# Optimization experiments

Measured on AMD Instinct MI355X. Metric: run time of the kernel, lower is better.

## Reference

```python
import jax, jax.numpy as jnp
import numpy as np

B, S, DIM = 2, 2048, 2048
NH, NKV = 32, 8
HD = DIM // NH  # 64


def setup_inputs() -> dict:
    key = jax.random.key(0)
    ks = jax.random.split(key, 6)
    x = jax.random.normal(ks[0], (B, S, DIM), jnp.float32)
    # realistic rotary tables: [S, HD//2]
    inv_freq = 1.0 / (10000.0 ** (jnp.arange(0, HD, 2, dtype=jnp.float32) / HD))
    freqs = jnp.arange(S, dtype=jnp.float32)[:, None] * inv_freq[None, :]
    cos, sin = jnp.cos(freqs), jnp.sin(freqs)
    init = lambda k, shape: jax.random.normal(k, shape, jnp.float32) * (shape[0] ** -0.5)
    Wq = init(ks[1], (DIM, NH * HD))
    Wk = init(ks[2], (DIM, NKV * HD))
    Wv = init(ks[3], (DIM, NKV * HD))
    Wo = init(ks[4], (NH * HD, DIM))
    return {"x": x, "cos": cos, "sin": sin, "Wq": Wq, "Wk": Wk, "Wv": Wv, "Wo": Wo}


def _rope(t, c, s):
    # t: [B, S, H, HD]; c, s: [1, S, 1, HD//2]; consecutive-pair (v1) style
    b, sl, h, hd = t.shape
    tp = t.reshape(b, sl, h, hd // 2, 2)
    t0, t1 = tp[..., 0], tp[..., 1]
    return jnp.stack([t0 * c - t1 * s, t0 * s + t1 * c], axis=-1).reshape(b, sl, h, hd)


def reference(x, cos, sin, Wq, Wk, Wv, Wo):
    b, sl, _ = x.shape
    q = (x @ Wq).reshape(b, sl, NH, HD)
    k = (x @ Wk).reshape(b, sl, NKV, HD)
    v = (x @ Wv).reshape(b, sl, NKV, HD)
    c = cos[None, :, None, :]
    s = sin[None, :, None, :]
    q = _rope(q, c, s)
    k = _rope(k, c, s)
    n_rep = NH // NKV
    k = jnp.repeat(k, n_rep, axis=2)  # GQA repeat_interleave over heads
    v = jnp.repeat(v, n_rep, axis=2)
    scale = 1.0 / np.sqrt(HD)
    scores = jnp.einsum("bqhd,bkhd->bhqk", q, k) * scale  # [B, H, S, S]
    causal = jnp.tril(jnp.ones((sl, sl), dtype=bool))
    scores = jnp.where(causal[None, None], scores, -jnp.inf)
    p = jax.nn.softmax(scores, axis=-1)
    out = jnp.einsum("bhqk,bkhd->bqhd", p, v).reshape(b, sl, NH * HD)
    return out @ Wo
```

## Files before the change

### kernel.cpp

```cpp
#include <hip/hip_runtime.h>
#include <hip/hip_bf16.h>


typedef __attribute__((ext_vector_type(8))) short short8;
typedef __attribute__((ext_vector_type(4))) float f32x4;
typedef __attribute__((ext_vector_type(16))) float f32x16;
typedef __attribute__((ext_vector_type(2))) int i32x2;
typedef __attribute__((ext_vector_type(4))) int i32x4;

__device__ __forceinline__ unsigned short f2bfu(float f){
  unsigned u = __float_as_uint(f);
  u += 0x7FFFu + ((u >> 16) & 1u);
  return (unsigned short)(u >> 16);
}
__device__ __forceinline__ float bfu2f(unsigned short u){
  return __uint_as_float(((unsigned)u) << 16);
}
__device__ __forceinline__ unsigned cvt_pk_bf16(float lo, float hi){
  unsigned r;
  asm("v_cvt_pk_bf16_f32 %0, %1, %2" : "=v"(r) : "v"(lo), "v"(hi));
  return r;
}
__device__ __forceinline__ i32x2 pl32swap(int a, int b){
  auto r = __builtin_amdgcn_permlane32_swap(a, b, false, false);
  return __builtin_bit_cast(i32x2, r);
}
__device__ __forceinline__ int swz64(int row, int slot){
  return row * 64 + (((slot) ^ (row & 7)) << 3);
}
template<int N> __device__ __forceinline__ void vm_wait(){
  if constexpr (N == 8)      asm volatile("s_waitcnt vmcnt(8)" ::: "memory");
  else if constexpr (N == 7) asm volatile("s_waitcnt vmcnt(7)" ::: "memory");
  else if constexpr (N == 6) asm volatile("s_waitcnt vmcnt(6)" ::: "memory");
  else if constexpr (N == 4) asm volatile("s_waitcnt vmcnt(4)" ::: "memory");
  else if constexpr (N == 3) asm volatile("s_waitcnt vmcnt(3)" ::: "memory");
  else if constexpr (N == 2) asm volatile("s_waitcnt vmcnt(2)" ::: "memory");
  else                       asm volatile("s_waitcnt vmcnt(0)" ::: "memory");
}

__global__ void convx_kernel(const float* __restrict__ x, unsigned short* __restrict__ xb, int n4){
  int i = blockIdx.x * blockDim.x + threadIdx.x;
  if (i >= n4) return;
  float4 v = reinterpret_cast<const float4*>(x)[i];
  ushort4 o;
  o.x = f2bfu(v.x); o.y = f2bfu(v.y); o.z = f2bfu(v.z); o.w = f2bfu(v.w);
  reinterpret_cast<ushort4*>(xb)[i] = o;
}

__global__ void transpose_conv_kernel(const float* __restrict__ in, unsigned short* __restrict__ out,
                                      int Min, int Nin){
  __shared__ float t[32][33];
  int c0 = blockIdx.x * 32, r0 = blockIdx.y * 32;
  int tx = threadIdx.x, ty = threadIdx.y;
  #pragma unroll
  for (int i = ty; i < 32; i += 8) t[i][tx] = in[(size_t)(r0 + i) * Nin + c0 + tx];
  __syncthreads();
  #pragma unroll
  for (int i = ty; i < 32; i += 8) out[(size_t)(c0 + i) * Min + r0 + tx] = f2bfu(t[tx][i]);
}

#define PH4(SLOT,KK,VMW,...) { \
  const unsigned short* sAc = &sA[SLOT][(KK)*8192]; \
  const unsigned short* sBc = &sB[SLOT][(KK)*RB]; \
  short8 afr[8]; short8 bfr[4]; \
  _Pragma("unroll") for (int m_ = 0; m_ < 8; m_++) \
    afr[m_] = *reinterpret_cast<const short8*>(sAc + aOff[m_]); \
  _Pragma("unroll") for (int n_ = 0; n_ < NF; n_++) \
    bfr[n_] = *reinterpret_cast<const short8*>(sBc + bOff[n_]); \
  __VA_ARGS__; \
  __builtin_amdgcn_s_barrier(); \
  asm volatile("s_waitcnt lgkmcnt(0)" ::: "memory"); \
  __builtin_amdgcn_sched_barrier(0); \
  __builtin_amdgcn_s_setprio(1); \
  _Pragma("unroll") for (int m_ = 0; m_ < 8; m_++){ \
    _Pragma("unroll") for (int n_ = 0; n_ < NF; n_++){ \
      acc[m_][n_] = __builtin_amdgcn_mfma_f32_16x16x32_bf16(afr[m_], bfr[n_], acc[m_][n_], 0, 0, 0); }} \
  __builtin_amdgcn_s_setprio(0); \
  VMW; \
  __builtin_amdgcn_s_barrier(); \
}

template<int NF, bool OUTBF16>
__global__ __launch_bounds__(512, 2) void gemm4p_kernel(const unsigned short* __restrict__ A,
                                                        const unsigned short* __restrict__ B,
                                                        void* __restrict__ Cp,
                                                        int M, int N, int K, int nbx){
  constexpr int RB  = NF * 2048;
  constexpr int VMS = (NF == 4) ? 8 : (NF == 3 ? 7 : 6);
  __shared__ unsigned short sA[2][16384];
  __shared__ unsigned short sB[2][2 * RB];
  const int tid = threadIdx.x;
  const int l = tid & 63, w = tid >> 6;
  const int quad = l >> 4, c16 = l & 15;
  const int cpx = (int)gridDim.x >> 3;
  const int id2 = ((int)blockIdx.x & 7) * cpx + ((int)blockIdx.x >> 3);
  const int bx = id2 % nbx, by = id2 / nbx;
  const int row0 = by * 256, col0 = bx * (NF * 64);
  const int wr = w >> 2, wc = w & 3;

  const int rlA0 = w * 32 + (l >> 2), rlA1 = rlA0 + 16;
  const unsigned short* gA0 = A + (size_t)(row0 + rlA0) * K + (((l & 3) ^ ((rlA0 >> 1) & 3)) << 3);
  const unsigned short* gA1 = A + (size_t)(row0 + rlA1) * K + (((l & 3) ^ ((rlA1 >> 1) & 3)) << 3);
  const unsigned short* gB0;
  const unsigned short* gB1 = nullptr;
  const unsigned short* gB2 = nullptr;
  if constexpr (NF == 4){
    gB0 = B + (size_t)(col0 + rlA0) * K + (((l & 3) ^ ((rlA0 >> 1) & 3)) << 3);
    gB1 = B + (size_t)(col0 + rlA1) * K + (((l & 3) ^ ((rlA1 >> 1) & 3)) << 3);
  } else {
    const int rlB0 = w * 16 + (l >> 2);
    gB0 = B + (size_t)(col0 + rlB0) * K + (((l & 3) ^ ((rlB0 >> 1) & 3)) << 3);
    if constexpr (NF == 3){
      const int rlB2 = 128 + (w & 3) * 16 + (l >> 2);
      gB2 = B + (size_t)(col0 + rlB2) * K + (((l & 3) ^ ((rlB2 >> 1) & 3)) << 3);
    }
  }

  auto stA = [&](int slot, int kk, int col){
    __builtin_amdgcn_global_load_lds((const __attribute__((address_space(1))) void*)(gA0 + col),
        (__attribute__((address_space(3))) void*)(&sA[slot][kk * 8192 + w * 1024]), 16, 0, 0);
    __builtin_amdgcn_global_load_lds((const __attribute__((address_space(1))) void*)(gA1 + col),
        (__attribute__((address_space(3))) void*)(&sA[slot][kk * 8192 + w * 1024 + 512]), 16, 0, 0);
  };
  auto stB = [&](int slot, int kk, int col){
    if constexpr (NF == 4){
      __builtin_amdgcn_global_load_lds((const __attribute__((address_space(1))) void*)(gB0 + col),
          (__attribute__((address_space(3))) void*)(&sB[slot][kk * RB + w * 1024]), 16, 0, 0);
      __builtin_amdgcn_global_load_lds((const __attribute__((address_space(1))) void*)(gB1 + col),
          (__attribute__((address_space(3))) void*)(&sB[slot][kk * RB + w * 1024 + 512]), 16, 0, 0);
    } else if constexpr (NF == 3){
      __builtin_amdgcn_global_load_lds((const __attribute__((address_space(1))) void*)(gB0 + col),
          (__attribute__((address_space(3))) void*)(&sB[slot][kk * RB + w * 512]), 16, 0, 0);
      if ((kk == 0) ? (w < 4) : (w >= 4))
        __builtin_amdgcn_global_load_lds((const __attribute__((address_space(1))) void*)(gB2 + col),
            (__attribute__((address_space(3))) void*)(&sB[slot][kk * RB + 4096 + (w & 3) * 512]), 16, 0, 0);
    } else {
      __builtin_amdgcn_global_load_lds((const __attribute__((address_space(1))) void*)(gB0 + col),
          (__attribute__((address_space(3))) void*)(&sB[slot][kk * RB + w * 512]), 16, 0, 0);
    }
  };

  int aOff[8], bOff[4];
  #pragma unroll
  for (int mf = 0; mf < 8; mf++){
    int row = wr * 128 + mf * 16 + c16;
    aOff[mf] = row * 32 + ((quad ^ ((row >> 1) & 3)) << 3);
  }
  #pragma unroll
  for (int nf = 0; nf < 4; nf++){
    int row = wc * (NF * 16) + nf * 16 + c16;
    bOff[nf] = row * 32 + ((quad ^ ((row >> 1) & 3)) << 3);
  }

  stA(0, 0, 0);  stB(0, 0, 0);
  stA(0, 1, 32); stB(0, 1, 32);
  stA(1, 0, 64); stB(1, 0, 64);
  vm_wait<VMS>();
  __builtin_amdgcn_s_barrier();

  f32x4 acc[8][4] = {};
  const int NI = K >> 7;
  #pragma unroll 1
  for (int j = 0; j < NI - 1; ++j){
    const int t1c  = (2 * j + 1) * 64 + 32;
    const int t2c0 = (2 * j + 2) * 64;
    const int t2c1 = t2c0 + 32;
    const int t3c0 = (2 * j + 3) * 64;
    PH4(0,0, vm_wait<VMS>(), stA(1,1,t1c);  stB(1,1,t1c))
    PH4(0,1, vm_wait<VMS>(), stA(0,0,t2c0); stB(0,0,t2c0))
    PH4(1,0, vm_wait<VMS>(), stA(0,1,t2c1); stB(0,1,t2c1))
    PH4(1,1, vm_wait<VMS>(), stA(1,0,t3c0); stB(1,0,t3c0))
  }
  {
    const int t1c = K - 32;
    PH4(0,0, vm_wait<VMS>(), stA(1,1,t1c); stB(1,1,t1c))
    PH4(0,1, vm_wait<0>(), ;)
    PH4(1,0, vm_wait<0>(), ;)
    PH4(1,1, (void)0, ;)
  }

  #pragma unroll
  for (int mf = 0; mf < 8; mf++)
    #pragma unroll
    for (int nf = 0; nf < NF; nf++)
      #pragma unroll
      for (int r = 0; r < 4; r++){
        size_t off = (size_t)(row0 + wr * 128 + mf * 16 + quad * 4 + r) * N + (col0 + wc * (NF * 16) + nf * 16 + c16);
        if (OUTBF16) ((unsigned short*)Cp)[off] = f2bfu(acc[mf][nf][r]);
        else         ((float*)Cp)[off] = acc[mf][nf][r];
      }
}

__global__ void rope_kernel(const unsigned short* __restrict__ qkv, const float* __restrict__ cosb,
                            const float* __restrict__ sinb, unsigned short* __restrict__ Qo,
                            unsigned short* __restrict__ Ko){
  int idx = blockIdx.x * 256 + threadIdx.x;
  const int NQ = 4096 * 1024;
  if (idx < NQ){
    int m = idx >> 10, p = idx & 1023;
    int h = p >> 5, i = p & 31;
    int s = m & 2047;
    unsigned pr = *reinterpret_cast<const unsigned*>(qkv + (size_t)m * 3072 + h * 64 + 2 * i);
    float t0 = bfu2f((unsigned short)(pr & 0xFFFFu));
    float t1 = bfu2f((unsigned short)(pr >> 16));
    float c = cosb[s * 32 + i], sn = sinb[s * 32 + i];
    const float SC = 0.18033688011112042f;
    float o0 = (t0 * c - t1 * sn) * SC;
    float o1 = (t0 * sn + t1 * c) * SC;
    unsigned ow = (unsigned)f2bfu(o0) | ((unsigned)f2bfu(o1) << 16);
    *reinterpret_cast<unsigned*>(Qo + (size_t)m * 2048 + h * 64 + 2 * i) = ow;
  } else {
    int j = idx - NQ;
    int m = j >> 8, p = j & 255;
    int kvh = p >> 5, i = p & 31;
    int s = m & 2047, b = m >> 11;
    unsigned pr = *reinterpret_cast<const unsigned*>(qkv + (size_t)m * 3072 + 2048 + kvh * 64 + 2 * i);
    float t0 = bfu2f((unsigned short)(pr & 0xFFFFu));
    float t1 = bfu2f((unsigned short)(pr >> 16));
    float c = cosb[s * 32 + i], sn = sinb[s * 32 + i];
    float o0 = t0 * c - t1 * sn;
    float o1 = t0 * sn + t1 * c;
    unsigned ow = (unsigned)f2bfu(o0) | ((unsigned)f2bfu(o1) << 16);
    *reinterpret_cast<unsigned*>(Ko + ((size_t)(b * 8 + kvh) * 2048 + s) * 64 + 2 * i) = ow;
  }
}

__global__ void vtrans_kernel(const unsigned short* __restrict__ qkv, unsigned short* __restrict__ Vt){
  __shared__ float t[64][65];
  int bh = blockIdx.y;
  int s0 = blockIdx.x * 64;
  int b = bh >> 3, kvh = bh & 7;
  int tid = threadIdx.x;
  #pragma unroll
  for (int it = 0; it < 16; it++){
    int id = it * 256 + tid;
    int sl = id >> 6, d = id & 63;
    unsigned short u = qkv[(size_t)(b * 2048 + s0 + sl) * 3072 + 2560 + kvh * 64 + d];
    t[sl][d] = bfu2f(u);
  }
  __syncthreads();
  #pragma unroll
  for (int it = 0; it < 16; it++){
    int id = it * 256 + tid;
    int dl = id >> 6, sl = id & 63;
    Vt[((size_t)(b * 8 + kvh) * 64 + dl) * 2048 + s0 + sl] = f2bfu(t[sl][dl]);
  }
}

__global__ __launch_bounds__(256) void attn_kernel(const unsigned short* __restrict__ Q,
                                                   const unsigned short* __restrict__ Kt,
                                                   const unsigned short* __restrict__ Vt,
                                                   unsigned short* __restrict__ O){
  __shared__ unsigned short sK[2][64 * 64];
  __shared__ unsigned short sV[2][64 * 64];
  const int tid = threadIdx.x;
  const int l = tid & 63, w = tid >> 6;
  const int q32 = l & 31, hi = l >> 5;
  const int bid = blockIdx.x;
  const int qt = 15 - (bid >> 6);
  const int bh = bid & 63;
  const int b = bh >> 5, h = bh & 31, kvh = h >> 2;
  const int q0w = qt * 128 + w * 32;
  const int nt = 2 * qt + 2;

  const unsigned short* Kb = Kt + (size_t)(b * 8 + kvh) * 2048 * 64;
  const unsigned short* Vb = Vt + (size_t)(b * 8 + kvh) * 64 * 2048;

  auto stage = [&](int kv0, int buf){
    #pragma unroll
    for (int c = 0; c < 2; c++){
      const int rl = w * 16 + c * 8 + (l >> 3);
      const int ce = (((l & 7) ^ (l >> 3)) << 3);
      __builtin_amdgcn_global_load_lds(
        (const __attribute__((address_space(1))) void*)(Kb + (size_t)(kv0 + rl) * 64 + ce),
        (__attribute__((address_space(3))) void*)(&sK[buf][(w * 16 + c * 8) * 64]), 16, 0, 0);
      __builtin_amdgcn_global_load_lds(
        (const __attribute__((address_space(1))) void*)(Vb + (size_t)rl * 2048 + kv0 + ce),
        (__attribute__((address_space(3))) void*)(&sV[buf][(w * 16 + c * 8) * 64]), 16, 0, 0);
    }
  };

  short8 qv[4];
  {
    const unsigned short* Qp = Q + (size_t)(b * 2048 + q0w + q32) * 2048 + h * 64 + hi * 8;
    #pragma unroll
    for (int kd = 0; kd < 4; kd++) qv[kd] = *reinterpret_cast<const short8*>(Qp + kd * 16);
  }

  const short8 ones = {0x3F80, 0x3F80, 0x3F80, 0x3F80, 0x3F80, 0x3F80, 0x3F80, 0x3F80};

  f32x16 accA = {}, accB = {};
  f32x16 accl = {};
  float m_run = -1e30f;

#define MKAP(Z, R0, AP) { \
    unsigned A_ = cvt_pk_bf16(Z[R0+0], Z[R0+1]); \
    unsigned B_ = cvt_pk_bf16(Z[R0+2], Z[R0+3]); \
    unsigned C_ = cvt_pk_bf16(Z[R0+4], Z[R0+5]); \
    unsigned D_ = cvt_pk_bf16(Z[R0+6], Z[R0+7]); \
    i32x2 s1_ = pl32swap((int)A_, (int)C_); \
    i32x2 s2_ = pl32swap((int)B_, (int)D_); \
    i32x4 q_ = {s1_[0], s2_[0], s1_[1], s2_[1]}; \
    AP = __builtin_bit_cast(short8, q_); \
  }

  stage(0, 0);
  vm_wait<0>();
  __builtin_amdgcn_s_barrier();

  for (int t = 0; t < nt; ++t){
    const int kv0 = t * 64;
    const int buf = t & 1;
    if (t + 1 < nt) stage((t + 1) * 64, buf ^ 1);

    const unsigned short* sKc = &sK[buf][0];
    const unsigned short* sVc = &sV[buf][0];

    f32x16 z0 = {}, z1 = {};
    __builtin_amdgcn_s_setprio(1);
    #pragma unroll
    for (int kd = 0; kd < 4; kd++){
      const int u = kd * 2 + hi;
      short8 ak0 = *reinterpret_cast<const short8*>(&sKc[swz64(q32, u)]);
      short8 ak1 = *reinterpret_cast<const short8*>(&sKc[swz64(32 + q32, u)]);
      z0 = __builtin_amdgcn_mfma_f32_32x32x16_bf16(ak0, qv[kd], z0, 0, 0, 0);
      z1 = __builtin_amdgcn_mfma_f32_32x32x16_bf16(ak1, qv[kd], z1, 0, 0, 0);
    }
    __builtin_amdgcn_s_setprio(0);

    if (kv0 + 63 > q0w){
      const int qg = q0w + q32;
      #pragma unroll
      for (int r = 0; r < 16; r++){
        const int kr = (r & 3) + 8 * (r >> 2) + 4 * hi;
        if (kv0 + kr > qg)      z0[r] = -1e30f;
        if (kv0 + 32 + kr > qg) z1[r] = -1e30f;
      }
    }

    float tm = fmaxf(z0[0], z0[1]);
    #pragma unroll
    for (int r = 2; r < 16; r++) tm = fmaxf(tm, z0[r]);
    #pragma unroll
    for (int r = 0; r < 16; r++) tm = fmaxf(tm, z1[r]);
    tm = fmaxf(tm, __shfl_xor(tm, 32));

    if (!__all(tm <= m_run + 8.0f)){
      float mn = fmaxf(m_run, tm);
      float al = __builtin_amdgcn_exp2f(m_run - mn);
      m_run = mn;
      #pragma unroll
      for (int r = 0; r < 16; r++){
        const int qrow = (r & 3) + 8 * (r >> 2) + 4 * hi;
        float alr = __shfl(al, qrow);
        accA[r] *= alr; accB[r] *= alr; accl[r] *= alr;
      }
    }

    #pragma unroll
    for (int r = 0; r < 16; r++){
      z0[r] = __builtin_amdgcn_exp2f(z0[r] - m_run);
      z1[r] = __builtin_amdgcn_exp2f(z1[r] - m_run);
    }

    short8 apA, apB;
    __builtin_amdgcn_s_setprio(1);
    MKAP(z0, 0, apA)
    MKAP(z0, 8, apB)
    accl = __builtin_amdgcn_mfma_f32_32x32x16_bf16(apA, ones, accl, 0, 0, 0);
    accl = __builtin_amdgcn_mfma_f32_32x32x16_bf16(apB, ones, accl, 0, 0, 0);
    {
      short8 bv;
      bv = *reinterpret_cast<const short8*>(&sVc[swz64(q32, 0 * 2 + hi)]);
      accA = __builtin_amdgcn_mfma_f32_32x32x16_bf16(apA, bv, accA, 0, 0, 0);
      bv = *reinterpret_cast<const short8*>(&sVc[swz64(q32, 1 * 2 + hi)]);
      accA = __builtin_amdgcn_mfma_f32_32x32x16_bf16(apB, bv, accA, 0, 0, 0);
      bv = *reinterpret_cast<const short8*>(&sVc[swz64(32 + q32, 0 * 2 + hi)]);
      accB = __builtin_amdgcn_mfma_f32_32x32x16_bf16(apA, bv, accB, 0, 0, 0);
      bv = *reinterpret_cast<const short8*>(&sVc[swz64(32 + q32, 1 * 2 + hi)]);
      accB = __builtin_amdgcn_mfma_f32_32x32x16_bf16(apB, bv, accB, 0, 0, 0);
    }
    MKAP(z1, 0, apA)
    MKAP(z1, 8, apB)
    accl = __builtin_amdgcn_mfma_f32_32x32x16_bf16(apA, ones, accl, 0, 0, 0);
    accl = __builtin_amdgcn_mfma_f32_32x32x16_bf16(apB, ones, accl, 0, 0, 0);
    {
      short8 bv;
      bv = *reinterpret_cast<const short8*>(&sVc[swz64(q32, 2 * 2 + hi)]);
      accA = __builtin_amdgcn_mfma_f32_32x32x16_bf16(apA, bv, accA, 0, 0, 0);
      bv = *reinterpret_cast<const short8*>(&sVc[swz64(q32, 3 * 2 + hi)]);
      accA = __builtin_amdgcn_mfma_f32_32x32x16_bf16(apB, bv, accA, 0, 0, 0);
      bv = *reinterpret_cast<const short8*>(&sVc[swz64(32 + q32, 2 * 2 + hi)]);
      accB = __builtin_amdgcn_mfma_f32_32x32x16_bf16(apA, bv, accB, 0, 0, 0);
      bv = *reinterpret_cast<const short8*>(&sVc[swz64(32 + q32, 3 * 2 + hi)]);
      accB = __builtin_amdgcn_mfma_f32_32x32x16_bf16(apB, bv, accB, 0, 0, 0);
    }
    __builtin_amdgcn_s_setprio(0);

    vm_wait<0>();
    __builtin_amdgcn_s_barrier();
  }
#undef MKAP

  #pragma unroll
  for (int r = 0; r < 16; r++){
    const float inv = 1.0f / accl[r];
    const int qrow = q0w + (r & 3) + 8 * (r >> 2) + 4 * hi;
    const size_t base = (size_t)(b * 2048 + qrow) * 2048 + h * 64 + q32;
    O[base]      = f2bfu(accA[r] * inv);
    O[base + 32] = f2bfu(accB[r] * inv);
  }
}

extern "C" void kernel_launch(void* const* d_in, const int* in_sizes, int n_in,
                              void* d_out, int out_size, void* d_ws, size_t ws_size,
                              hipStream_t stream){
  (void)in_sizes; (void)n_in; (void)out_size; (void)ws_size;
  const float* x  = (const float*)d_in[0];
  const float* cb = (const float*)d_in[1];
  const float* sb = (const float*)d_in[2];
  const float* Wq = (const float*)d_in[3];
  const float* Wk = (const float*)d_in[4];
  const float* Wv = (const float*)d_in[5];
  const float* Wo = (const float*)d_in[6];
  float* out = (float*)d_out;
  char* ws = (char*)d_ws;

  unsigned short* qkv = (unsigned short*)(ws + 0);
  unsigned short* xb  = (unsigned short*)(ws + 25165824);
  unsigned short* wt  = (unsigned short*)(ws + 41943040);
  unsigned short* qb  = (unsigned short*)(ws + 54525952);
  unsigned short* kb  = (unsigned short*)(ws + 71303168);
  unsigned short* vt  = (unsigned short*)(ws + 75497472);

  dim3 tb(32, 8);
  convx_kernel<<<8192, 256, 0, stream>>>(x, xb, 2097152);
  transpose_conv_kernel<<<dim3(64, 64), tb, 0, stream>>>(Wq, wt, 2048, 2048);
  transpose_conv_kernel<<<dim3(16, 64), tb, 0, stream>>>(Wk, wt + (size_t)2048 * 2048, 2048, 512);
  transpose_conv_kernel<<<dim3(16, 64), tb, 0, stream>>>(Wv, wt + (size_t)2560 * 2048, 2048, 512);
  gemm4p_kernel<3, true><<<256, 512, 0, stream>>>(xb, wt, qkv, 4096, 3072, 2048, 16);
  rope_kernel<<<20480, 256, 0, stream>>>(qkv, cb, sb, qb, kb);
  vtrans_kernel<<<dim3(32, 16), 256, 0, stream>>>(qkv, vt);
  transpose_conv_kernel<<<dim3(64, 64), tb, 0, stream>>>(Wo, wt, 2048, 2048);
  attn_kernel<<<1024, 256, 0, stream>>>(qb, kb, vt, xb);
  gemm4p_kernel<2, false><<<256, 512, 0, stream>>>(xb, wt, out, 4096, 2048, 2048, 16);
}
```

Baseline: 202.0 us.

## Load K/V tiles directly from global memory instead of LDS double-buffering

Removes the shared-memory double-buffered staging of K and V, including the barriers and vmcnt waits. Each wave now reads its K and V fragments straight from global memory, relying on the cache for reuse across the 4 waves and across blocks that share a KV head. Per-wave tile counts are now computed from each wave's own query range, so waves skip causal tiles they do not need once barriers are gone. The max reduction is also restructured into a tree. The cost is exposed global-load latency with no prefetch and redundant cache traffic, since each wave fetches the same K/V rows.

```diff
diff --git a/kernel.cpp b/kernel.cpp
--- a/kernel.cpp
+++ b/kernel.cpp
@@ -24,9 +24,6 @@
 __device__ __forceinline__ i32x2 pl32swap(int a, int b){
   auto r = __builtin_amdgcn_permlane32_swap(a, b, false, false);
   return __builtin_bit_cast(i32x2, r);
-}
-__device__ __forceinline__ int swz64(int row, int slot){
-  return row * 64 + (((slot) ^ (row & 7)) << 3);
 }
 template<int N> __device__ __forceinline__ void vm_wait(){
   if constexpr (N == 8)      asm volatile("s_waitcnt vmcnt(8)" ::: "memory");
@@ -251,8 +248,6 @@
                                                    const unsigned short* __restrict__ Kt,
                                                    const unsigned short* __restrict__ Vt,
                                                    unsigned short* __restrict__ O){
-  __shared__ unsigned short sK[2][64 * 64];
-  __shared__ unsigned short sV[2][64 * 64];
   const int tid = threadIdx.x;
   const int l = tid & 63, w = tid >> 6;
   const int q32 = l & 31, hi = l >> 5;
@@ -261,24 +256,10 @@
   const int bh = bid & 63;
   const int b = bh >> 5, h = bh & 31, kvh = h >> 2;
   const int q0w = qt * 128 + w * 32;
-  const int nt = 2 * qt + 2;
+  const int nt = ((q0w + 31) >> 6) + 1;
 
   const unsigned short* Kb = Kt + (size_t)(b * 8 + kvh) * 2048 * 64;
   const unsigned short* Vb = Vt + (size_t)(b * 8 + kvh) * 64 * 2048;
-
-  auto stage = [&](int kv0, int buf){
-    #pragma unroll
-    for (int c = 0; c < 2; c++){
-      const int rl = w * 16 + c * 8 + (l >> 3);
-      const int ce = (((l & 7) ^ (l >> 3)) << 3);
-      __builtin_amdgcn_global_load_lds(
-        (const __attribute__((address_space(1))) void*)(Kb + (size_t)(kv0 + rl) * 64 + ce),
-        (__attribute__((address_space(3))) void*)(&sK[buf][(w * 16 + c * 8) * 64]), 16, 0, 0);
-      __builtin_amdgcn_global_load_lds(
-        (const __attribute__((address_space(1))) void*)(Vb + (size_t)rl * 2048 + kv0 + ce),
-        (__attribute__((address_space(3))) void*)(&sV[buf][(w * 16 + c * 8) * 64]), 16, 0, 0);
-    }
-  };
 
   short8 qv[4];
   {
@@ -292,6 +273,9 @@
   f32x16 accA = {}, accB = {};
   f32x16 accl = {};
   float m_run = -1e30f;
+
+  const unsigned short* Vr0b = Vb + (size_t)q32 * 2048 + hi * 8;
+  const unsigned short* Vr1b = Vr0b + (size_t)32 * 2048;
 
 #define MKAP(Z, R0, AP) { \
     unsigned A_ = cvt_pk_bf16(Z[R0+0], Z[R0+1]); \
@@ -304,25 +288,17 @@
     AP = __builtin_bit_cast(short8, q_); \
   }
 
-  stage(0, 0);
-  vm_wait<0>();
-  __builtin_amdgcn_s_barrier();
-
   for (int t = 0; t < nt; ++t){
     const int kv0 = t * 64;
-    const int buf = t & 1;
-    if (t + 1 < nt) stage((t + 1) * 64, buf ^ 1);
-
-    const unsigned short* sKc = &sK[buf][0];
-    const unsigned short* sVc = &sV[buf][0];
-
+
+    const unsigned short* Kr0 = Kb + (size_t)(kv0 + q32) * 64 + hi * 8;
+    const unsigned short* Kr1 = Kr0 + 32 * 64;
     f32x16 z0 = {}, z1 = {};
     __builtin_amdgcn_s_setprio(1);
     #pragma unroll
     for (int kd = 0; kd < 4; kd++){
-      const int u = kd * 2 + hi;
-      short8 ak0 = *reinterpret_cast<const short8*>(&sKc[swz64(q32, u)]);
-      short8 ak1 = *reinterpret_cast<const short8*>(&sKc[swz64(32 + q32, u)]);
+      short8 ak0 = *reinterpret_cast<const short8*>(Kr0 + kd * 16);
+      short8 ak1 = *reinterpret_cast<const short8*>(Kr1 + kd * 16);
       z0 = __builtin_amdgcn_mfma_f32_32x32x16_bf16(ak0, qv[kd], z0, 0, 0, 0);
       z1 = __builtin_amdgcn_mfma_f32_32x32x16_bf16(ak1, qv[kd], z1, 0, 0, 0);
     }
@@ -338,11 +314,12 @@
       }
     }
 
-    float tm = fmaxf(z0[0], z0[1]);
+    float m8[8];
     #pragma unroll
-    for (int r = 2; r < 16; r++) tm = fmaxf(tm, z0[r]);
-    #pragma unroll
-    for (int r = 0; r < 16; r++) tm = fmaxf(tm, z1[r]);
+    for (int r = 0; r < 8; r++) m8[r] = fmaxf(fmaxf(z0[r], z0[r + 8]), fmaxf(z1[r], z1[r + 8]));
+    float m4a = fmaxf(m8[0], m8[4]), m4b = fmaxf(m8[1], m8[5]);
+    float m4c = fmaxf(m8[2], m8[6]), m4d = fmaxf(m8[3], m8[7]);
+    float tm = fmaxf(fmaxf(m4a, m4b), fmaxf(m4c, m4d));
     tm = fmaxf(tm, __shfl_xor(tm, 32));
 
     if (!__all(tm <= m_run + 8.0f)){
@@ -363,6 +340,8 @@
       z1[r] = __builtin_amdgcn_exp2f(z1[r] - m_run);
     }
 
+    const unsigned short* Vr0 = Vr0b + kv0;
+    const unsigned short* Vr1 = Vr1b + kv0;
     short8 apA, apB;
     __builtin_amdgcn_s_setprio(1);
     MKAP(z0, 0, apA)
@@ -371,13 +350,13 @@
     accl = __builtin_amdgcn_mfma_f32_32x32x16_bf16(apB, ones, accl, 0, 0, 0);
     {
       short8 bv;
-      bv = *reinterpret_cast<const short8*>(&sVc[swz64(q32, 0 * 2 + hi)]);
+      bv = *reinterpret_cast<const short8*>(Vr0);
       accA = __builtin_amdgcn_mfma_f32_32x32x16_bf16(apA, bv, accA, 0, 0, 0);
-      bv = *reinterpret_cast<const short8*>(&sVc[swz64(q32, 1 * 2 + hi)]);
+      bv = *reinterpret_cast<const short8*>(Vr0 + 16);
       accA = __builtin_amdgcn_mfma_f32_32x32x16_bf16(apB, bv, accA, 0, 0, 0);
-      bv = *reinterpret_cast<const short8*>(&sVc[swz64(32 + q32, 0 * 2 + hi)]);
+      bv = *reinterpret_cast<const short8*>(Vr1);
       accB = __builtin_amdgcn_mfma_f32_32x32x16_bf16(apA, bv, accB, 0, 0, 0);
-      bv = *reinterpret_cast<const short8*>(&sVc[swz64(32 + q32, 1 * 2 + hi)]);
+      bv = *reinterpret_cast<const short8*>(Vr1 + 16);
       accB = __builtin_amdgcn_mfma_f32_32x32x16_bf16(apB, bv, accB, 0, 0, 0);
     }
     MKAP(z1, 0, apA)
@@ -386,19 +365,16 @@
     accl = __builtin_amdgcn_mfma_f32_32x32x16_bf16(apB, ones, accl, 0, 0, 0);
     {
       short8 bv;
-      bv = *reinterpret_cast<const short8*>(&sVc[swz64(q32, 2 * 2 + hi)]);
+      bv = *reinterpret_cast<const short8*>(Vr0 + 32);
       accA = __builtin_amdgcn_mfma_f32_32x32x16_bf16(apA, bv, accA, 0, 0, 0);
-      bv = *reinterpret_cast<const short8*>(&sVc[swz64(q32, 3 * 2 + hi)]);
+      bv = *reinterpret_cast<const short8*>(Vr0 + 48);
       accA = __builtin_amdgcn_mfma_f32_32x32x16_bf16(apB, bv, accA, 0, 0, 0);
-      bv = *reinterpret_cast<const short8*>(&sVc[swz64(32 + q32, 2 * 2 + hi)]);
+      bv = *reinterpret_cast<const short8*>(Vr1 + 32);
       accB = __builtin_amdgcn_mfma_f32_32x32x16_bf16(apA, bv, accB, 0, 0, 0);
-      bv = *reinterpret_cast<const short8*>(&sVc[swz64(32 + q32, 3 * 2 + hi)]);
+      bv = *reinterpret_cast<const short8*>(Vr1 + 48);
       accB = __builtin_amdgcn_mfma_f32_32x32x16_bf16(apB, bv, accB, 0, 0, 0);
     }
     __builtin_amdgcn_s_setprio(0);
-
-    vm_wait<0>();
-    __builtin_amdgcn_s_barrier();
   }
 #undef MKAP
 
```

Result: slower. 264.4 us (+30.9%).
